# Optimization experiments

Hardware: AMD Instinct MI355X
Metric: run time of the kernel (lower is better)

Reference implementation:

```python
import jax, jax.numpy as jnp
import numpy as np

V, E, H, O = 32000, 512, 1024, 8   # vocab, embed_dim, hidden_dim, output_dim
B, T = 64, 512
PAD = 1  # padding_idx=1 in nn.Embedding


def setup_inputs() -> dict:
    key = jax.random.key(0)
    ks = jax.random.split(key, 8)
    s = 1.0 / np.sqrt(H)  # torch LSTM init scale
    x = jax.random.randint(ks[0], (B, T), 0, V)
    W_emb = jax.random.normal(ks[1], (V, E), dtype=jnp.float32)
    W_emb = W_emb.at[PAD].set(0.0)  # padding row is zero
    W_ih = jax.random.uniform(ks[2], (4 * H, E), jnp.float32, -s, s)
    W_hh = jax.random.uniform(ks[3], (4 * H, H), jnp.float32, -s, s)
    b_ih = jax.random.uniform(ks[4], (4 * H,), jnp.float32, -s, s)
    b_hh = jax.random.uniform(ks[5], (4 * H,), jnp.float32, -s, s)
    W_out = jax.random.uniform(ks[6], (O, H), jnp.float32, -s, s)
    b_out = jax.random.uniform(ks[7], (O,), jnp.float32, -s, s)
    return {"x": x, "W_emb": W_emb, "W_ih": W_ih, "W_hh": W_hh,
            "b_ih": b_ih, "b_hh": b_hh, "W_out": W_out, "b_out": b_out}


def _lstm_scan(emb_tbe, W_ih, W_hh, b_ih, b_hh):
    # emb_tbe: [T, B, E] -> hidden states [T, B, H]; torch gate order i,f,g,o
    Hh = W_hh.shape[1]
    b = b_ih + b_hh

    def step(carry, x_t):
        h, c = carry
        z = x_t @ W_ih.T + h @ W_hh.T + b  # [B, 4H]
        i, f, g, o = jnp.split(z, 4, axis=-1)
        c = jax.nn.sigmoid(f) * c + jax.nn.sigmoid(i) * jnp.tanh(g)
        h = jax.nn.sigmoid(o) * jnp.tanh(c)
        return (h, c), h

    h0 = jnp.zeros((emb_tbe.shape[1], Hh), emb_tbe.dtype)
    _, hs = jax.lax.scan(step, (h0, h0), emb_tbe)
    return hs


def reference(x, W_emb, W_ih, W_hh, b_ih, b_hh, W_out, b_out):
    Bsz = x.shape[0]
    emb = W_emb[x]                                   # [B, T, E]
    hs = _lstm_scan(emb.transpose(1, 0, 2), W_ih, W_hh, b_ih, b_hh)
    outputs = hs.transpose(1, 0, 2)                  # [B, T, H]
    pad = (x == PAD)
    outputs = jnp.where(pad[..., None], 0.0, outputs)  # masked_fill_
    lengths = jnp.sum(~pad, axis=1)                  # non-pad token counts
    final = outputs[jnp.arange(Bsz), lengths - 1]    # [B, H]
    # Dropout(p=0.5) is identity in eval mode
    logits = final @ W_out.T + b_out                 # [B, O]
    return logits
```

## Files before the change

kernel.cpp:

```cpp
#include <hip/hip_runtime.h>

typedef short bf16x8 __attribute__((ext_vector_type(8)));
typedef float f32x4  __attribute__((ext_vector_type(4)));
typedef unsigned long long u64;

#define MFMA16(a, b, c) __builtin_amdgcn_mfma_f32_16x16x32_bf16((a), (b), (c), 0, 0, 0)
#define AT_LD(p, o)    __hip_atomic_load((p), (o), __HIP_MEMORY_SCOPE_AGENT)
#define AT_ST(p, v, o) __hip_atomic_store((p), (v), (o), __HIP_MEMORY_SCOPE_AGENT)
#define AT_ADD(p, v, o) __hip_atomic_fetch_add((p), (v), (o), __HIP_MEMORY_SCOPE_AGENT)

#define HSLOT 67584

__device__ __forceinline__ unsigned short f2bf(float f) {
  union { float f; unsigned u; } v; v.f = f;
  unsigned u = v.u;
  u += 0x7fffu + ((u >> 16) & 1u);
  return (unsigned short)(u >> 16);
}
__device__ __forceinline__ float bf2f(unsigned short h) {
  union { unsigned u; float f; } v; v.u = ((unsigned)h) << 16;
  return v.f;
}
__device__ __forceinline__ float sigf(float x) { return 1.f / (1.f + __expf(-x)); }
__device__ __forceinline__ float tanh_(float x) {
  x = fminf(15.f, fmaxf(-15.f, x));
  float e = __expf(2.f * x);
  return (e - 1.f) / (e + 1.f);
}

__device__ __forceinline__ void gbar_rec(unsigned* bar, int wg, unsigned target) {
  __syncthreads();
  if (threadIdx.x == 0) {
    asm volatile("" ::: "memory");
    unsigned arr = AT_ADD(bar + (wg & 3) * 64, 1u, __ATOMIC_RELAXED);
    if (arr == target * 32u - 1u) {
      unsigned rarr = AT_ADD(bar + 256, 1u, __ATOMIC_RELAXED);
      if (rarr == target * 4u - 1u) AT_ST(bar + 320, target, __ATOMIC_RELAXED);
    }
    while (AT_LD(bar + 320, __ATOMIC_RELAXED) < target) __builtin_amdgcn_s_sleep(1);
    asm volatile("" ::: "memory");
  }
  __syncthreads();
}

__device__ __forceinline__ void gbar_gemm(unsigned* bar, unsigned target) {
  __syncthreads();
  if (threadIdx.x == 0) {
    unsigned arr = AT_ADD(bar + 384, 1u, __ATOMIC_RELEASE);
    if (arr == target * 128u - 1u) AT_ST(bar + 448, target, __ATOMIC_RELEASE);
    while (AT_LD(bar + 448, __ATOMIC_RELAXED) < target) __builtin_amdgcn_s_sleep(4);
    asm volatile("" ::: "memory");
  }
  __syncthreads();
}

__global__ void k_conv(const float* __restrict__ wih, const float* __restrict__ whh,
                       const float* __restrict__ wemb,
                       unsigned short* __restrict__ oih, unsigned short* __restrict__ ohh,
                       unsigned short* __restrict__ oemb) {
  const size_t NIH = (size_t)4096 * 512, NHH = (size_t)4096 * 1024;
  const size_t NE = (size_t)32000 * 512;
  size_t i0 = ((size_t)blockIdx.x * blockDim.x + threadIdx.x) * 4;
  size_t gs = (size_t)gridDim.x * blockDim.x * 4;
  for (size_t j = i0; j < NIH; j += gs) {
    float4 v = *(const float4*)(wih + j);
    uint2 pk;
    pk.x = (unsigned)f2bf(v.x) | ((unsigned)f2bf(v.y) << 16);
    pk.y = (unsigned)f2bf(v.z) | ((unsigned)f2bf(v.w) << 16);
    *(uint2*)(oih + j) = pk;
  }
  for (size_t j = i0; j < NHH; j += gs) {
    float4 v = *(const float4*)(whh + j);
    uint2 pk;
    pk.x = (unsigned)f2bf(v.x) | ((unsigned)f2bf(v.y) << 16);
    pk.y = (unsigned)f2bf(v.z) | ((unsigned)f2bf(v.w) << 16);
    *(uint2*)(ohh + j) = pk;
  }
  if (oemb)
    for (size_t j = i0; j < NE; j += gs) {
      float4 v = *(const float4*)(wemb + j);
      uint2 pk;
      pk.x = (unsigned)f2bf(v.x) | ((unsigned)f2bf(v.y) << 16);
      pk.y = (unsigned)f2bf(v.z) | ((unsigned)f2bf(v.w) << 16);
      *(uint2*)(oemb + j) = pk;
    }
}

__global__ void k_tsel(const int* __restrict__ x, int* __restrict__ tsel,
                       int* __restrict__ padsel) {
  int b = threadIdx.x >> 3, j = threadIdx.x & 7;
  int c = 0;
  for (int t = j * 64; t < j * 64 + 64; ++t) c += (x[b * 512 + t] != 1) ? 1 : 0;
  c += __shfl_xor(c, 1);
  c += __shfl_xor(c, 2);
  c += __shfl_xor(c, 4);
  if (j == 0) {
    int ts = (c - 1) & 511;
    tsel[b] = ts;
    padsel[b] = (x[b * 512 + ts] == 1) ? 1 : 0;
  }
}

__global__ void k_logits(const float* __restrict__ finalb, const float* __restrict__ Wout,
                         const float* __restrict__ bout, float* __restrict__ out) {
  int tid = threadIdx.x;
  for (int e = tid; e < 512; e += 256) {
    int b = e >> 3, o = e & 7;
    const float* f = finalb + (size_t)b * 1024;
    const float* w = Wout + (size_t)o * 1024;
    float s = 0.f;
    for (int k = 0; k < 1024; ++k) s += f[k] * w[k];
    out[e] = s + bout[o];
  }
}

struct SmemT {
  unsigned short sW[32][1032];
  union {
    struct { unsigned short A[128][72]; unsigned short Bt[256][72]; } g;
    struct { float z[64][33]; } rec;
    struct { unsigned short zs[128][136]; } zst;
  } u;
};

__global__ __launch_bounds__(256, 1) void k_main(
    const int* __restrict__ x, const float* __restrict__ Wemb,
    const float* __restrict__ bih, const float* __restrict__ bhh,
    const unsigned short* __restrict__ Wihb, const unsigned short* __restrict__ Whhb,
    const unsigned short* __restrict__ wembb,
    unsigned short* __restrict__ hr, float* __restrict__ finalb,
    const int* __restrict__ tsel, const int* __restrict__ padsel,
    unsigned short* __restrict__ zxr, unsigned* __restrict__ bar, int chunkT,
    int fullzx) {
  __shared__ SmemT smem;
  const int wg = blockIdx.x, tid = threadIdx.x;
  const int wave = tid >> 6, lane = tid & 63;
  const int l15 = lane & 15, lg = lane >> 4;
  unsigned* gemm_done = bar + 512;
  unsigned* rec_done  = bar + 576;

  const f32x4 fz = {0.f, 0.f, 0.f, 0.f};
  const int nChunks = 512 / chunkT;
  const size_t slotE = (size_t)chunkT * 64 * 4096;

  if (wg < 128) {
    for (int e = tid; e < 32 * 128; e += 256) {
      int n = e >> 7;
      int kq = (e & 127) << 3;
      int grow = (n >> 3) * 1024 + wg * 8 + (n & 7);
      *(uint4*)&smem.sW[n][kq] = *(const uint4*)(Whhb + (size_t)grow * 1024 + kq);
    }
    const int q = tid & 3;
    const int my_b = tid >> 2;
    const int zc = wg * 8 + 2 * q;
    float biasv[4][2];
#pragma unroll
    for (int g = 0; g < 4; ++g)
#pragma unroll
      for (int c = 0; c < 2; ++c) biasv[g][c] = bih[g * 1024 + zc + c] + bhh[g * 1024 + zc + c];
    const int my_tsel = tsel[my_b];
    const int my_pad = padsel[my_b];
    const size_t hwe = (size_t)((my_b >> 4) * 32 + (wg >> 2)) * 512 +
                       (size_t)(wg & 3) * 128 + (size_t)(my_b & 15) * 8 + 2 * q;
    float cc0 = 0.f, cc1 = 0.f;
    unsigned bt = 0;

    AT_ST((unsigned*)hr + (wg * 256 + tid), 0u, __ATOMIC_RELAXED);
    gbar_rec(bar, wg, ++bt);

    for (int ch = 0; ch < nChunks; ++ch) {
      const int t0 = ch * chunkT;
      const unsigned short* zxbase =
          zxr + (fullzx ? (size_t)ch * slotE : (size_t)(ch & 1) * slotE);

      if (tid == 0) {
        while (AT_LD(gemm_done, __ATOMIC_RELAXED) < (unsigned)(ch + 1))
          __builtin_amdgcn_s_sleep(4);
        (void)AT_LD(gemm_done, __ATOMIC_ACQUIRE);
        asm volatile("" ::: "memory");
      }
      __syncthreads();

      union { uint2 u2[2]; unsigned short s[8]; } vv;
      {
        const unsigned short* zr = zxbase + (size_t)my_b * 4096 + zc * 4;
        vv.u2[0] = *(const uint2*)zr;
        vv.u2[1] = *(const uint2*)(zr + 4);
      }

      for (int tl = 0; tl < chunkT; ++tl) {
        const int t = t0 + tl;

        const unsigned short* hp =
            hr + (size_t)(t & 15) * HSLOT + (size_t)wave * 16384 + (size_t)lane * 8;
        f32x4 r0 = fz, r1 = fz;
        bf16x8 af[32];
#pragma unroll
        for (int j = 0; j < 32; ++j) af[j] = *(const bf16x8*)(hp + (size_t)j * 512);
#pragma unroll
        for (int j = 0; j < 32; ++j) {
          int ks = j * 32;
          bf16x8 b0 = *(const bf16x8*)&smem.sW[l15][ks + (lg << 3)];
          bf16x8 b1 = *(const bf16x8*)&smem.sW[16 + l15][ks + (lg << 3)];
          r0 = MFMA16(af[j], b0, r0);
          r1 = MFMA16(af[j], b1, r1);
        }
#pragma unroll
        for (int r = 0; r < 4; ++r) {
          smem.u.rec.z[wave * 16 + (lg << 2) + r][l15] = r0[r];
          smem.u.rec.z[wave * 16 + (lg << 2) + r][16 + l15] = r1[r];
        }
        __syncthreads();

        int hc = 2 * q;
        float zi0 = smem.u.rec.z[my_b][hc]          + biasv[0][0] + bf2f(vv.s[0]);
        float zf0 = smem.u.rec.z[my_b][8 + hc]      + biasv[1][0] + bf2f(vv.s[1]);
        float zg0 = smem.u.rec.z[my_b][16 + hc]     + biasv[2][0] + bf2f(vv.s[2]);
        float zo0 = smem.u.rec.z[my_b][24 + hc]     + biasv[3][0] + bf2f(vv.s[3]);
        float zi1 = smem.u.rec.z[my_b][hc + 1]      + biasv[0][1] + bf2f(vv.s[4]);
        float zf1 = smem.u.rec.z[my_b][8 + hc + 1]  + biasv[1][1] + bf2f(vv.s[5]);
        float zg1 = smem.u.rec.z[my_b][16 + hc + 1] + biasv[2][1] + bf2f(vv.s[6]);
        float zo1 = smem.u.rec.z[my_b][24 + hc + 1] + biasv[3][1] + bf2f(vv.s[7]);

        cc0 = sigf(zf0) * cc0 + sigf(zi0) * tanh_(zg0);
        cc1 = sigf(zf1) * cc1 + sigf(zi1) * tanh_(zg1);
        float h0 = sigf(zo0) * tanh_(cc0);
        float h1 = sigf(zo1) * tanh_(cc1);

        if (t == my_tsel) {
          finalb[(size_t)my_b * 1024 + zc]     = my_pad ? 0.f : h0;
          finalb[(size_t)my_b * 1024 + zc + 1] = my_pad ? 0.f : h1;
        }
        unsigned hp32 = (unsigned)f2bf(h0) | ((unsigned)f2bf(h1) << 16);
        AT_ST((unsigned*)(hr + (size_t)((t + 1) & 15) * HSLOT + hwe), hp32,
              __ATOMIC_RELAXED);

        if (tl + 1 < chunkT) {
          const unsigned short* zn =
              zxbase + (size_t)((tl + 1) * 64 + my_b) * 4096 + zc * 4;
          vv.u2[0] = *(const uint2*)zn;
          vv.u2[1] = *(const uint2*)(zn + 4);
        }
        gbar_rec(bar, wg, ++bt);
      }
      if (!fullzx && wg == 0 && tid == 0)
        AT_ST(rec_done, (unsigned)(ch + 1), __ATOMIC_RELAXED);
    }
  } else {
    const int gw = wg - 128;
    unsigned gt = 0;
    for (int ch = 0; ch < nChunks; ++ch) {
      if (!fullzx && tid == 0 && ch >= 2) {
        while (AT_LD(rec_done, __ATOMIC_RELAXED) < (unsigned)(ch - 1))
          __builtin_amdgcn_s_sleep(4);
        asm volatile("" ::: "memory");
      }
      __syncthreads();

      const int t0 = ch * chunkT;
      unsigned short* zx = zxr + (fullzx ? (size_t)ch * slotE : (size_t)(ch & 1) * slotE);
      const int pmN = chunkT >> 1;
      const int npatch = pmN * 16;

      for (int p = gw; p < npatch; p += 128) {
        const int pm = p % pmN;
        const int n0 = (p / pmN) * 256;
        f32x4 acc[8][4];
#pragma unroll
        for (int mt = 0; mt < 8; ++mt)
#pragma unroll
          for (int nt = 0; nt < 4; ++nt) acc[mt][nt] = fz;

        for (int kc = 0; kc < 512; kc += 64) {
          __syncthreads();
          {
            int r = tid >> 1, half = (tid & 1) << 5;
            int tl = pm * 2 + (r >> 6), b = r & 63;
            int erow = x[b * 512 + t0 + tl];
            if (wembb) {
              const unsigned short* srcp = wembb + (size_t)erow * 512 + kc + half;
#pragma unroll
              for (int j = 0; j < 32; j += 8)
                *(uint4*)&smem.u.g.A[r][half + j] = *(const uint4*)(srcp + j);
            } else {
              const float* srcp = Wemb + (size_t)erow * 512 + kc + half;
#pragma unroll
              for (int j = 0; j < 32; j += 4) {
                float4 v = *(const float4*)(srcp + j);
                uint2 pk;
                pk.x = (unsigned)f2bf(v.x) | ((unsigned)f2bf(v.y) << 16);
                pk.y = (unsigned)f2bf(v.z) | ((unsigned)f2bf(v.w) << 16);
                *(uint2*)&smem.u.g.A[r][half + j] = pk;
              }
            }
          }
          {
            int zcx = n0 + tid;
            int wrow = (zcx & 3) * 1024 + (zcx >> 2);
            const unsigned short* srcp = Wihb + (size_t)wrow * 512 + kc;
#pragma unroll
            for (int j = 0; j < 64; j += 8)
              *(uint4*)&smem.u.g.Bt[tid][j] = *(const uint4*)(srcp + j);
          }
          __syncthreads();
#pragma unroll
          for (int ks = 0; ks < 64; ks += 32) {
            bf16x8 af[8];
#pragma unroll
            for (int mt = 0; mt < 8; ++mt)
              af[mt] = *(const bf16x8*)&smem.u.g.A[mt * 16 + l15][ks + (lg << 3)];
#pragma unroll
            for (int nt = 0; nt < 4; ++nt) {
              bf16x8 bfr =
                  *(const bf16x8*)&smem.u.g.Bt[(wave * 4 + nt) * 16 + l15][ks + (lg << 3)];
#pragma unroll
              for (int mt = 0; mt < 8; ++mt)
                acc[mt][nt] = MFMA16(af[mt], bfr, acc[mt][nt]);
            }
          }
        }
#pragma unroll
        for (int h = 0; h < 2; ++h) {
          __syncthreads();
          if ((wave >> 1) == h) {
#pragma unroll
            for (int mt = 0; mt < 8; ++mt)
#pragma unroll
              for (int nt = 0; nt < 4; ++nt)
#pragma unroll
                for (int r = 0; r < 4; ++r)
                  smem.u.zst.zs[mt * 16 + (lg << 2) + r][(wave & 1) * 64 + nt * 16 + l15] =
                      f2bf(acc[mt][nt][r]);
          }
          __syncthreads();
          int m = tid >> 1, qq = (tid & 1) << 6;
          int tl2 = pm * 2 + (m >> 6), bb = m & 63;
          unsigned short* dst = zx + ((size_t)(tl2 * 64 + bb)) * 4096 + n0 + h * 128 + qq;
#pragma unroll
          for (int j = 0; j < 64; j += 8)
            *(uint4*)(dst + j) = *(const uint4*)&smem.u.zst.zs[m][qq + j];
        }
      }
      gbar_gemm(bar, ++gt);
      if (wg == 128 && tid == 0) AT_ST(gemm_done, gt, __ATOMIC_RELAXED);
    }
  }
}

extern "C" void kernel_launch(void* const* d_in, const int* in_sizes, int n_in,
                              void* d_out, int out_size, void* d_ws, size_t ws_size,
                              hipStream_t stream) {
  (void)in_sizes; (void)n_in; (void)out_size;
  const int*   x    = (const int*)  d_in[0];
  const float* Wemb = (const float*)d_in[1];
  const float* Wih  = (const float*)d_in[2];
  const float* Whh  = (const float*)d_in[3];
  const float* bih  = (const float*)d_in[4];
  const float* bhh  = (const float*)d_in[5];
  const float* Wout = (const float*)d_in[6];
  const float* bout = (const float*)d_in[7];
  float* out = (float*)d_out;
  char* ws = (char*)d_ws;

  constexpr size_t OFF_WIH = 0;
  constexpr size_t OFF_WHH = OFF_WIH + (size_t)4096 * 512 * 2;
  constexpr size_t OFF_HR  = OFF_WHH + (size_t)4096 * 1024 * 2;
  constexpr size_t OFF_FIN = OFF_HR + (size_t)16 * HSLOT * 2;
  constexpr size_t OFF_TS  = OFF_FIN + (size_t)64 * 1024 * 4;
  constexpr size_t OFF_PS  = OFF_TS + 4096;
  constexpr size_t OFF_BAR = OFF_PS + 4096;
  constexpr size_t OFF_WEB = OFF_BAR + 4096;
  constexpr size_t WEB_SZ  = (size_t)32000 * 512 * 2;
  constexpr size_t ZX_FULL = (size_t)512 * 64 * 4096 * 2;

  int chunkT = 16;
  bool wbf = true;
  int fullzx = 0;
  if (OFF_WEB + WEB_SZ + ZX_FULL <= ws_size) {
    fullzx = 1;
  } else if (OFF_WEB + WEB_SZ + (size_t)2 * 16 * 64 * 4096 * 2 <= ws_size) {
  } else if (OFF_WEB + (size_t)2 * 16 * 64 * 4096 * 2 <= ws_size) {
    wbf = false;
  } else {
    wbf = false;
    while (chunkT > 2 &&
           OFF_WEB + (size_t)2 * chunkT * 64 * 4096 * 2 > ws_size)
      chunkT >>= 1;
  }
  const size_t OFF_ZX = OFF_WEB + (wbf ? WEB_SZ : 0);

  unsigned short* wihb  = (unsigned short*)(ws + OFF_WIH);
  unsigned short* whhb  = (unsigned short*)(ws + OFF_WHH);
  unsigned short* hr    = (unsigned short*)(ws + OFF_HR);
  float* finalb         = (float*)(ws + OFF_FIN);
  int* tsel             = (int*)(ws + OFF_TS);
  int* padsel           = (int*)(ws + OFF_PS);
  unsigned* bar         = (unsigned*)(ws + OFF_BAR);
  unsigned short* wembb = wbf ? (unsigned short*)(ws + OFF_WEB) : (unsigned short*)nullptr;
  unsigned short* zxr   = (unsigned short*)(ws + OFF_ZX);

  hipMemsetAsync(ws + OFF_BAR, 0, 4096, stream);
  k_conv<<<2048, 256, 0, stream>>>(Wih, Whh, Wemb, wihb, whhb, wembb);
  k_tsel<<<1, 512, 0, stream>>>(x, tsel, padsel);
  k_main<<<256, 256, 0, stream>>>(x, Wemb, bih, bhh, wihb, whhb, wembb, hr, finalb,
                                  tsel, padsel, zxr, bar, chunkT, fullzx);
  k_logits<<<1, 256, 0, stream>>>(finalb, Wout, bout, out);
}
```

Before: 3.322 ms.

## Split input GEMM into separate kernel and use flag-based recurrence barrier

When the workspace can hold the full input-projection buffer, the embedding×W_ih GEMM now runs as its own 256-block kernel ahead of a dedicated 128-block recurrence kernel, replacing the fused producer/consumer kernel. The recurrence uses a new barrier in which each block writes a per-block flag and block 0 gathers them and publishes a generation counter, replacing the hierarchical atomic-add barrier. An acquire load is issued only once every 16 steps. This aims to cut per-step barrier latency and remove GEMM interference with the serial recurrence, at the cost of losing overlap between the GEMM and the recurrence and relying on weak memory ordering.

```diff
diff --git a/kernel.cpp b/kernel.cpp
--- a/kernel.cpp
+++ b/kernel.cpp
@@ -26,6 +26,33 @@
   x = fminf(15.f, fmaxf(-15.f, x));
   float e = __expf(2.f * x);
   return (e - 1.f) / (e + 1.f);
+}
+
+__device__ __forceinline__ void flagbar(unsigned* bar, int wg, unsigned target,
+                                        int do_acq) {
+  unsigned* gen = bar + 8192;
+  __syncthreads();
+  if (threadIdx.x == 0) {
+    asm volatile("" ::: "memory");
+    AT_ST(bar + wg * 64, target, __ATOMIC_RELAXED);
+  }
+  if (wg == 0) {
+    if (threadIdx.x < 128) {
+      while (AT_LD(bar + threadIdx.x * 64, __ATOMIC_RELAXED) < target)
+        __builtin_amdgcn_s_sleep(1);
+    }
+    __syncthreads();
+    if (threadIdx.x == 0) AT_ST(gen, target, __ATOMIC_RELAXED);
+  } else {
+    if (threadIdx.x == 0) {
+      while (AT_LD(gen, __ATOMIC_RELAXED) < target) __builtin_amdgcn_s_sleep(1);
+    }
+  }
+  if (do_acq && threadIdx.x == 0) {
+    (void)AT_LD(gen, __ATOMIC_ACQUIRE);
+    asm volatile("" ::: "memory");
+  }
+  __syncthreads();
 }
 
 __device__ __forceinline__ void gbar_rec(unsigned* bar, int wg, unsigned target) {
@@ -42,7 +69,6 @@
   }
   __syncthreads();
 }
-
 __device__ __forceinline__ void gbar_gemm(unsigned* bar, unsigned target) {
   __syncthreads();
   if (threadIdx.x == 0) {
@@ -114,6 +140,211 @@
   }
 }
 
+struct GSmem {
+  union {
+    struct { unsigned short A[128][72]; unsigned short Bt[256][72]; } g;
+    struct { unsigned short zs[128][136]; } zst;
+  } u;
+  unsigned short pad[14336];
+};
+
+__global__ __launch_bounds__(256, 1) void k_gemm(
+    const int* __restrict__ x, const float* __restrict__ Wemb,
+    const unsigned short* __restrict__ Wihb, const unsigned short* __restrict__ wembb,
+    unsigned short* __restrict__ zxr) {
+  __shared__ GSmem smem;
+  const int wg = blockIdx.x, tid = threadIdx.x;
+  const int wave = tid >> 6, lane = tid & 63;
+  const int l15 = lane & 15, lg = lane >> 4;
+  if (tid == 65535) smem.pad[0] = 0;
+  const f32x4 fz = {0.f, 0.f, 0.f, 0.f};
+  const int pmN = 256, npatch = pmN * 16;
+
+  for (int p = wg; p < npatch; p += 256) {
+    const int pm = p % pmN;
+    const int n0 = (p / pmN) * 256;
+    f32x4 acc[8][4];
+#pragma unroll
+    for (int mt = 0; mt < 8; ++mt)
+#pragma unroll
+      for (int nt = 0; nt < 4; ++nt) acc[mt][nt] = fz;
+
+    for (int kc = 0; kc < 512; kc += 64) {
+      __syncthreads();
+      {
+        int r = tid >> 1, half = (tid & 1) << 5;
+        int t = pm * 2 + (r >> 6), b = r & 63;
+        int erow = x[b * 512 + t];
+        if (wembb) {
+          const unsigned short* srcp = wembb + (size_t)erow * 512 + kc + half;
+#pragma unroll
+          for (int j = 0; j < 32; j += 8)
+            *(uint4*)&smem.u.g.A[r][half + j] = *(const uint4*)(srcp + j);
+        } else {
+          const float* srcp = Wemb + (size_t)erow * 512 + kc + half;
+#pragma unroll
+          for (int j = 0; j < 32; j += 4) {
+            float4 v = *(const float4*)(srcp + j);
+            uint2 pk;
+            pk.x = (unsigned)f2bf(v.x) | ((unsigned)f2bf(v.y) << 16);
+            pk.y = (unsigned)f2bf(v.z) | ((unsigned)f2bf(v.w) << 16);
+            *(uint2*)&smem.u.g.A[r][half + j] = pk;
+          }
+        }
+      }
+      {
+        int zcx = n0 + tid;
+        int wrow = (zcx & 3) * 1024 + (zcx >> 2);
+        const unsigned short* srcp = Wihb + (size_t)wrow * 512 + kc;
+#pragma unroll
+        for (int j = 0; j < 64; j += 8)
+          *(uint4*)&smem.u.g.Bt[tid][j] = *(const uint4*)(srcp + j);
+      }
+      __syncthreads();
+#pragma unroll
+      for (int ks = 0; ks < 64; ks += 32) {
+        bf16x8 af[8];
+#pragma unroll
+        for (int mt = 0; mt < 8; ++mt)
+          af[mt] = *(const bf16x8*)&smem.u.g.A[mt * 16 + l15][ks + (lg << 3)];
+#pragma unroll
+        for (int nt = 0; nt < 4; ++nt) {
+          bf16x8 bfr =
+              *(const bf16x8*)&smem.u.g.Bt[(wave * 4 + nt) * 16 + l15][ks + (lg << 3)];
+#pragma unroll
+          for (int mt = 0; mt < 8; ++mt)
+            acc[mt][nt] = MFMA16(af[mt], bfr, acc[mt][nt]);
+        }
+      }
+    }
+#pragma unroll
+    for (int h = 0; h < 2; ++h) {
+      __syncthreads();
+      if ((wave >> 1) == h) {
+#pragma unroll
+        for (int mt = 0; mt < 8; ++mt)
+#pragma unroll
+          for (int nt = 0; nt < 4; ++nt)
+#pragma unroll
+            for (int r = 0; r < 4; ++r)
+              smem.u.zst.zs[mt * 16 + (lg << 2) + r][(wave & 1) * 64 + nt * 16 + l15] =
+                  f2bf(acc[mt][nt][r]);
+      }
+      __syncthreads();
+      int m = tid >> 1, qq = (tid & 1) << 6;
+      int t2 = pm * 2 + (m >> 6), bb = m & 63;
+      unsigned short* dst = zxr + ((size_t)(t2 * 64 + bb)) * 4096 + n0 + h * 128 + qq;
+#pragma unroll
+      for (int j = 0; j < 64; j += 8)
+        *(uint4*)(dst + j) = *(const uint4*)&smem.u.zst.zs[m][qq + j];
+    }
+  }
+}
+
+struct RSmem {
+  unsigned short sW[32][1032];
+  float z[64][33];
+  unsigned short pad[5120];
+};
+
+__global__ __launch_bounds__(256, 1) void k_rec(
+    const float* __restrict__ bih, const float* __restrict__ bhh,
+    const unsigned short* __restrict__ Whhb,
+    unsigned short* __restrict__ hr, float* __restrict__ finalb,
+    const int* __restrict__ tsel, const int* __restrict__ padsel,
+    const unsigned short* __restrict__ zxr, unsigned* __restrict__ bar) {
+  __shared__ RSmem smem;
+  const int wg = blockIdx.x, tid = threadIdx.x;
+  const int wave = tid >> 6, lane = tid & 63;
+  const int l15 = lane & 15, lg = lane >> 4;
+  if (tid == 65535) smem.pad[0] = 0;
+  const f32x4 fz = {0.f, 0.f, 0.f, 0.f};
+
+  for (int e = tid; e < 32 * 128; e += 256) {
+    int n = e >> 7, kq = (e & 127) << 3;
+    int grow = (n >> 3) * 1024 + wg * 8 + (n & 7);
+    *(uint4*)&smem.sW[n][kq] = *(const uint4*)(Whhb + (size_t)grow * 1024 + kq);
+  }
+  const int q = tid & 3;
+  const int my_b = tid >> 2;
+  const int zc = wg * 8 + 2 * q;
+  float biasv[4][2];
+#pragma unroll
+  for (int g = 0; g < 4; ++g)
+#pragma unroll
+    for (int c = 0; c < 2; ++c)
+      biasv[g][c] = bih[g * 1024 + zc + c] + bhh[g * 1024 + zc + c];
+  const int my_tsel = tsel[my_b];
+  const int my_pad = padsel[my_b];
+  const size_t hwe = (size_t)((my_b >> 4) * 32 + (wg >> 2)) * 512 +
+                     (size_t)(wg & 3) * 128 + (size_t)(my_b & 15) * 8 + 2 * q;
+  float cc0 = 0.f, cc1 = 0.f;
+  unsigned bt = 0;
+
+  AT_ST((unsigned*)hr + (wg * 256 + tid), 0u, __ATOMIC_RELAXED);
+  flagbar(bar, wg, ++bt, 0);
+
+  union { uint2 u2[2]; unsigned short s[8]; } vv;
+  {
+    const unsigned short* zr = zxr + (size_t)my_b * 4096 + zc * 4;
+    vv.u2[0] = *(const uint2*)zr;
+    vv.u2[1] = *(const uint2*)(zr + 4);
+  }
+
+  for (int t = 0; t < 512; ++t) {
+    const unsigned short* hp =
+        hr + (size_t)(t & 15) * HSLOT + (size_t)wave * 16384 + (size_t)lane * 8;
+    f32x4 r0 = fz, r1 = fz;
+    bf16x8 af[32];
+#pragma unroll
+    for (int j = 0; j < 32; ++j) af[j] = *(const bf16x8*)(hp + (size_t)j * 512);
+#pragma unroll
+    for (int j = 0; j < 32; ++j) {
+      int ks = j * 32;
+      bf16x8 b0 = *(const bf16x8*)&smem.sW[l15][ks + (lg << 3)];
+      bf16x8 b1 = *(const bf16x8*)&smem.sW[16 + l15][ks + (lg << 3)];
+      r0 = MFMA16(af[j], b0, r0);
+      r1 = MFMA16(af[j], b1, r1);
+    }
+#pragma unroll
+    for (int r = 0; r < 4; ++r) {
+      smem.z[wave * 16 + (lg << 2) + r][l15] = r0[r];
+      smem.z[wave * 16 + (lg << 2) + r][16 + l15] = r1[r];
+    }
+    __syncthreads();
+
+    int hc = 2 * q;
+    float zi0 = smem.z[my_b][hc]          + biasv[0][0] + bf2f(vv.s[0]);
+    float zf0 = smem.z[my_b][8 + hc]      + biasv[1][0] + bf2f(vv.s[1]);
+    float zg0 = smem.z[my_b][16 + hc]     + biasv[2][0] + bf2f(vv.s[2]);
+    float zo0 = smem.z[my_b][24 + hc]     + biasv[3][0] + bf2f(vv.s[3]);
+    float zi1 = smem.z[my_b][hc + 1]      + biasv[0][1] + bf2f(vv.s[4]);
+    float zf1 = smem.z[my_b][8 + hc + 1]  + biasv[1][1] + bf2f(vv.s[5]);
+    float zg1 = smem.z[my_b][16 + hc + 1] + biasv[2][1] + bf2f(vv.s[6]);
+    float zo1 = smem.z[my_b][24 + hc + 1] + biasv[3][1] + bf2f(vv.s[7]);
+
+    cc0 = sigf(zf0) * cc0 + sigf(zi0) * tanh_(zg0);
+    cc1 = sigf(zf1) * cc1 + sigf(zi1) * tanh_(zg1);
+    float h0 = sigf(zo0) * tanh_(cc0);
+    float h1 = sigf(zo1) * tanh_(cc1);
+
+    if (t == my_tsel) {
+      finalb[(size_t)my_b * 1024 + zc]     = my_pad ? 0.f : h0;
+      finalb[(size_t)my_b * 1024 + zc + 1] = my_pad ? 0.f : h1;
+    }
+    unsigned hp32 = (unsigned)f2bf(h0) | ((unsigned)f2bf(h1) << 16);
+    AT_ST((unsigned*)(hr + (size_t)((t + 1) & 15) * HSLOT + hwe), hp32,
+          __ATOMIC_RELAXED);
+
+    if (t + 1 < 512) {
+      const unsigned short* zn = zxr + ((size_t)(t + 1) * 64 + my_b) * 4096 + zc * 4;
+      vv.u2[0] = *(const uint2*)zn;
+      vv.u2[1] = *(const uint2*)(zn + 4);
+    }
+    flagbar(bar, wg, ++bt, (t & 15) == 6);
+  }
+}
+
 struct SmemT {
   unsigned short sW[32][1032];
   union {
@@ -130,23 +361,20 @@
     const unsigned short* __restrict__ wembb,
     unsigned short* __restrict__ hr, float* __restrict__ finalb,
     const int* __restrict__ tsel, const int* __restrict__ padsel,
-    unsigned short* __restrict__ zxr, unsigned* __restrict__ bar, int chunkT,
-    int fullzx) {
+    unsigned short* __restrict__ zxr, unsigned* __restrict__ bar, int chunkT) {
   __shared__ SmemT smem;
   const int wg = blockIdx.x, tid = threadIdx.x;
   const int wave = tid >> 6, lane = tid & 63;
   const int l15 = lane & 15, lg = lane >> 4;
   unsigned* gemm_done = bar + 512;
   unsigned* rec_done  = bar + 576;
-
   const f32x4 fz = {0.f, 0.f, 0.f, 0.f};
   const int nChunks = 512 / chunkT;
   const size_t slotE = (size_t)chunkT * 64 * 4096;
 
   if (wg < 128) {
     for (int e = tid; e < 32 * 128; e += 256) {
-      int n = e >> 7;
-      int kq = (e & 127) << 3;
+      int n = e >> 7, kq = (e & 127) << 3;
       int grow = (n >> 3) * 1024 + wg * 8 + (n & 7);
       *(uint4*)&smem.sW[n][kq] = *(const uint4*)(Whhb + (size_t)grow * 1024 + kq);
     }
@@ -157,22 +385,20 @@
 #pragma unroll
     for (int g = 0; g < 4; ++g)
 #pragma unroll
-      for (int c = 0; c < 2; ++c) biasv[g][c] = bih[g * 1024 + zc + c] + bhh[g * 1024 + zc + c];
+      for (int c = 0; c < 2; ++c)
+        biasv[g][c] = bih[g * 1024 + zc + c] + bhh[g * 1024 + zc + c];
     const int my_tsel = tsel[my_b];
     const int my_pad = padsel[my_b];
     const size_t hwe = (size_t)((my_b >> 4) * 32 + (wg >> 2)) * 512 +
                        (size_t)(wg & 3) * 128 + (size_t)(my_b & 15) * 8 + 2 * q;
     float cc0 = 0.f, cc1 = 0.f;
     unsigned bt = 0;
-
     AT_ST((unsigned*)hr + (wg * 256 + tid), 0u, __ATOMIC_RELAXED);
     gbar_rec(bar, wg, ++bt);
 
     for (int ch = 0; ch < nChunks; ++ch) {
       const int t0 = ch * chunkT;
-      const unsigned short* zxbase =
-          zxr + (fullzx ? (size_t)ch * slotE : (size_t)(ch & 1) * slotE);
-
+      const unsigned short* zxbase = zxr + (size_t)(ch & 1) * slotE;
       if (tid == 0) {
         while (AT_LD(gemm_done, __ATOMIC_RELAXED) < (unsigned)(ch + 1))
           __builtin_amdgcn_s_sleep(4);
@@ -180,17 +406,14 @@
         asm volatile("" ::: "memory");
       }
       __syncthreads();
-
       union { uint2 u2[2]; unsigned short s[8]; } vv;
       {
         const unsigned short* zr = zxbase + (size_t)my_b * 4096 + zc * 4;
         vv.u2[0] = *(const uint2*)zr;
         vv.u2[1] = *(const uint2*)(zr + 4);
       }
-
       for (int tl = 0; tl < chunkT; ++tl) {
         const int t = t0 + tl;
-
         const unsigned short* hp =
             hr + (size_t)(t & 15) * HSLOT + (size_t)wave * 16384 + (size_t)lane * 8;
         f32x4 r0 = fz, r1 = fz;
@@ -211,7 +434,6 @@
           smem.u.rec.z[wave * 16 + (lg << 2) + r][16 + l15] = r1[r];
         }
         __syncthreads();
-
         int hc = 2 * q;
         float zi0 = smem.u.rec.z[my_b][hc]          + biasv[0][0] + bf2f(vv.s[0]);
         float zf0 = smem.u.rec.z[my_b][8 + hc]      + biasv[1][0] + bf2f(vv.s[1]);
@@ -221,12 +443,10 @@
         float zf1 = smem.u.rec.z[my_b][8 + hc + 1]  + biasv[1][1] + bf2f(vv.s[5]);
         float zg1 = smem.u.rec.z[my_b][16 + hc + 1] + biasv[2][1] + bf2f(vv.s[6]);
         float zo1 = smem.u.rec.z[my_b][24 + hc + 1] + biasv[3][1] + bf2f(vv.s[7]);
-
         cc0 = sigf(zf0) * cc0 + sigf(zi0) * tanh_(zg0);
         cc1 = sigf(zf1) * cc1 + sigf(zi1) * tanh_(zg1);
         float h0 = sigf(zo0) * tanh_(cc0);
         float h1 = sigf(zo1) * tanh_(cc1);
-
         if (t == my_tsel) {
           finalb[(size_t)my_b * 1024 + zc]     = my_pad ? 0.f : h0;
           finalb[(size_t)my_b * 1024 + zc + 1] = my_pad ? 0.f : h1;
@@ -234,7 +454,6 @@
         unsigned hp32 = (unsigned)f2bf(h0) | ((unsigned)f2bf(h1) << 16);
         AT_ST((unsigned*)(hr + (size_t)((t + 1) & 15) * HSLOT + hwe), hp32,
               __ATOMIC_RELAXED);
-
         if (tl + 1 < chunkT) {
           const unsigned short* zn =
               zxbase + (size_t)((tl + 1) * 64 + my_b) * 4096 + zc * 4;
@@ -243,25 +462,22 @@
         }
         gbar_rec(bar, wg, ++bt);
       }
-      if (!fullzx && wg == 0 && tid == 0)
-        AT_ST(rec_done, (unsigned)(ch + 1), __ATOMIC_RELAXED);
+      if (wg == 0 && tid == 0) AT_ST(rec_done, (unsigned)(ch + 1), __ATOMIC_RELAXED);
     }
   } else {
     const int gw = wg - 128;
     unsigned gt = 0;
     for (int ch = 0; ch < nChunks; ++ch) {
-      if (!fullzx && tid == 0 && ch >= 2) {
+      if (tid == 0 && ch >= 2) {
         while (AT_LD(rec_done, __ATOMIC_RELAXED) < (unsigned)(ch - 1))
           __builtin_amdgcn_s_sleep(4);
         asm volatile("" ::: "memory");
       }
       __syncthreads();
-
       const int t0 = ch * chunkT;
-      unsigned short* zx = zxr + (fullzx ? (size_t)ch * slotE : (size_t)(ch & 1) * slotE);
+      unsigned short* zx = zxr + (size_t)(ch & 1) * slotE;
       const int pmN = chunkT >> 1;
       const int npatch = pmN * 16;
-
       for (int p = gw; p < npatch; p += 128) {
         const int pm = p % pmN;
         const int n0 = (p / pmN) * 256;
@@ -270,7 +486,6 @@
         for (int mt = 0; mt < 8; ++mt)
 #pragma unroll
           for (int nt = 0; nt < 4; ++nt) acc[mt][nt] = fz;
-
         for (int kc = 0; kc < 512; kc += 64) {
           __syncthreads();
           {
@@ -369,23 +584,22 @@
   constexpr size_t OFF_TS  = OFF_FIN + (size_t)64 * 1024 * 4;
   constexpr size_t OFF_PS  = OFF_TS + 4096;
   constexpr size_t OFF_BAR = OFF_PS + 4096;
-  constexpr size_t OFF_WEB = OFF_BAR + 4096;
+  constexpr size_t OFF_WEB = OFF_BAR + 40960;
   constexpr size_t WEB_SZ  = (size_t)32000 * 512 * 2;
   constexpr size_t ZX_FULL = (size_t)512 * 64 * 4096 * 2;
 
+  bool split = (OFF_WEB + WEB_SZ + ZX_FULL <= ws_size);
   int chunkT = 16;
   bool wbf = true;
-  int fullzx = 0;
-  if (OFF_WEB + WEB_SZ + ZX_FULL <= ws_size) {
-    fullzx = 1;
-  } else if (OFF_WEB + WEB_SZ + (size_t)2 * 16 * 64 * 4096 * 2 <= ws_size) {
-  } else if (OFF_WEB + (size_t)2 * 16 * 64 * 4096 * 2 <= ws_size) {
-    wbf = false;
-  } else {
-    wbf = false;
-    while (chunkT > 2 &&
-           OFF_WEB + (size_t)2 * chunkT * 64 * 4096 * 2 > ws_size)
-      chunkT >>= 1;
+  if (!split) {
+    if (OFF_WEB + WEB_SZ + (size_t)2 * 16 * 64 * 4096 * 2 <= ws_size) {
+    } else if (OFF_WEB + (size_t)2 * 16 * 64 * 4096 * 2 <= ws_size) {
+      wbf = false;
+    } else {
+      wbf = false;
+      while (chunkT > 2 && OFF_WEB + (size_t)2 * chunkT * 64 * 4096 * 2 > ws_size)
+        chunkT >>= 1;
+    }
   }
   const size_t OFF_ZX = OFF_WEB + (wbf ? WEB_SZ : 0);
 
@@ -399,10 +613,15 @@
   unsigned short* wembb = wbf ? (unsigned short*)(ws + OFF_WEB) : (unsigned short*)nullptr;
   unsigned short* zxr   = (unsigned short*)(ws + OFF_ZX);
 
-  hipMemsetAsync(ws + OFF_BAR, 0, 4096, stream);
+  hipMemsetAsync(ws + OFF_BAR, 0, 40960, stream);
   k_conv<<<2048, 256, 0, stream>>>(Wih, Whh, Wemb, wihb, whhb, wembb);
   k_tsel<<<1, 512, 0, stream>>>(x, tsel, padsel);
-  k_main<<<256, 256, 0, stream>>>(x, Wemb, bih, bhh, wihb, whhb, wembb, hr, finalb,
-                                  tsel, padsel, zxr, bar, chunkT, fullzx);
+  if (split) {
+    k_gemm<<<256, 256, 0, stream>>>(x, Wemb, wihb, wembb, zxr);
+    k_rec<<<128, 256, 0, stream>>>(bih, bhh, whhb, hr, finalb, tsel, padsel, zxr, bar);
+  } else {
+    k_main<<<256, 256, 0, stream>>>(x, Wemb, bih, bhh, wihb, whhb, wembb, hr, finalb,
+                                    tsel, padsel, zxr, bar, chunkT);
+  }
   k_logits<<<1, 256, 0, stream>>>(finalb, Wout, bout, out);
 }
```

Measured after the change: 3.326 ms. Within noise of the previous version (+0.1%).

## Replace atomic-counter grid barrier with per-WG flags and ring of zx slots

Applied to the files above, without the earlier changes.

The recurrent-step grid barrier changes from a hierarchical atomic-add counter to per-workgroup flag stores. Workgroup 0 polls all 128 flags and then publishes a generation word that the other workgroups spin on. The input-projection buffer becomes a ring of up to 32 slots sized from the workspace, replacing the full-or-double-buffer choice, and the GEMM workgroups wait on rec_done only when the ring wraps. The goal is to cut per-timestep barrier latency and atomic contention, at the cost of a serial gather step through workgroup 0 and a larger barrier area.

```diff
diff --git a/kernel.cpp b/kernel.cpp
--- a/kernel.cpp
+++ b/kernel.cpp
@@ -28,17 +28,24 @@
   return (e - 1.f) / (e + 1.f);
 }
 
-__device__ __forceinline__ void gbar_rec(unsigned* bar, int wg, unsigned target) {
+__device__ __forceinline__ void flagbar(unsigned* bar, int wg, unsigned target) {
+  unsigned* gen = bar + 8192;
   __syncthreads();
   if (threadIdx.x == 0) {
     asm volatile("" ::: "memory");
-    unsigned arr = AT_ADD(bar + (wg & 3) * 64, 1u, __ATOMIC_RELAXED);
-    if (arr == target * 32u - 1u) {
-      unsigned rarr = AT_ADD(bar + 256, 1u, __ATOMIC_RELAXED);
-      if (rarr == target * 4u - 1u) AT_ST(bar + 320, target, __ATOMIC_RELAXED);
-    }
-    while (AT_LD(bar + 320, __ATOMIC_RELAXED) < target) __builtin_amdgcn_s_sleep(1);
-    asm volatile("" ::: "memory");
+    AT_ST(bar + wg * 64, target, __ATOMIC_RELAXED);
+  }
+  if (wg == 0) {
+    if (threadIdx.x < 128) {
+      while (AT_LD(bar + threadIdx.x * 64, __ATOMIC_RELAXED) < target)
+        __builtin_amdgcn_s_sleep(1);
+    }
+    __syncthreads();
+    if (threadIdx.x == 0) AT_ST(gen, target, __ATOMIC_RELAXED);
+  } else {
+    if (threadIdx.x == 0) {
+      while (AT_LD(gen, __ATOMIC_RELAXED) < target) __builtin_amdgcn_s_sleep(1);
+    }
   }
   __syncthreads();
 }
@@ -46,9 +53,9 @@
 __device__ __forceinline__ void gbar_gemm(unsigned* bar, unsigned target) {
   __syncthreads();
   if (threadIdx.x == 0) {
-    unsigned arr = AT_ADD(bar + 384, 1u, __ATOMIC_RELEASE);
-    if (arr == target * 128u - 1u) AT_ST(bar + 448, target, __ATOMIC_RELEASE);
-    while (AT_LD(bar + 448, __ATOMIC_RELAXED) < target) __builtin_amdgcn_s_sleep(4);
+    unsigned arr = AT_ADD(bar + 8256, 1u, __ATOMIC_RELEASE);
+    if (arr == target * 128u - 1u) AT_ST(bar + 8320, target, __ATOMIC_RELEASE);
+    while (AT_LD(bar + 8320, __ATOMIC_RELAXED) < target) __builtin_amdgcn_s_sleep(4);
     asm volatile("" ::: "memory");
   }
   __syncthreads();
@@ -131,22 +138,20 @@
     unsigned short* __restrict__ hr, float* __restrict__ finalb,
     const int* __restrict__ tsel, const int* __restrict__ padsel,
     unsigned short* __restrict__ zxr, unsigned* __restrict__ bar, int chunkT,
-    int fullzx) {
+    int nslot) {
   __shared__ SmemT smem;
   const int wg = blockIdx.x, tid = threadIdx.x;
   const int wave = tid >> 6, lane = tid & 63;
   const int l15 = lane & 15, lg = lane >> 4;
-  unsigned* gemm_done = bar + 512;
-  unsigned* rec_done  = bar + 576;
-
+  unsigned* gemm_done = bar + 8384;
+  unsigned* rec_done  = bar + 8448;
   const f32x4 fz = {0.f, 0.f, 0.f, 0.f};
   const int nChunks = 512 / chunkT;
   const size_t slotE = (size_t)chunkT * 64 * 4096;
 
   if (wg < 128) {
     for (int e = tid; e < 32 * 128; e += 256) {
-      int n = e >> 7;
-      int kq = (e & 127) << 3;
+      int n = e >> 7, kq = (e & 127) << 3;
       int grow = (n >> 3) * 1024 + wg * 8 + (n & 7);
       *(uint4*)&smem.sW[n][kq] = *(const uint4*)(Whhb + (size_t)grow * 1024 + kq);
     }
@@ -157,40 +162,35 @@
 #pragma unroll
     for (int g = 0; g < 4; ++g)
 #pragma unroll
-      for (int c = 0; c < 2; ++c) biasv[g][c] = bih[g * 1024 + zc + c] + bhh[g * 1024 + zc + c];
+      for (int c = 0; c < 2; ++c)
+        biasv[g][c] = bih[g * 1024 + zc + c] + bhh[g * 1024 + zc + c];
     const int my_tsel = tsel[my_b];
     const int my_pad = padsel[my_b];
     const size_t hwe = (size_t)((my_b >> 4) * 32 + (wg >> 2)) * 512 +
                        (size_t)(wg & 3) * 128 + (size_t)(my_b & 15) * 8 + 2 * q;
     float cc0 = 0.f, cc1 = 0.f;
     unsigned bt = 0;
-
     AT_ST((unsigned*)hr + (wg * 256 + tid), 0u, __ATOMIC_RELAXED);
-    gbar_rec(bar, wg, ++bt);
+    flagbar(bar, wg, ++bt);
 
     for (int ch = 0; ch < nChunks; ++ch) {
       const int t0 = ch * chunkT;
-      const unsigned short* zxbase =
-          zxr + (fullzx ? (size_t)ch * slotE : (size_t)(ch & 1) * slotE);
-
+      const unsigned short* zxbase = zxr + (size_t)(ch % nslot) * slotE;
       if (tid == 0) {
         while (AT_LD(gemm_done, __ATOMIC_RELAXED) < (unsigned)(ch + 1))
-          __builtin_amdgcn_s_sleep(4);
+          __builtin_amdgcn_s_sleep(2);
         (void)AT_LD(gemm_done, __ATOMIC_ACQUIRE);
         asm volatile("" ::: "memory");
       }
       __syncthreads();
-
       union { uint2 u2[2]; unsigned short s[8]; } vv;
       {
         const unsigned short* zr = zxbase + (size_t)my_b * 4096 + zc * 4;
         vv.u2[0] = *(const uint2*)zr;
         vv.u2[1] = *(const uint2*)(zr + 4);
       }
-
       for (int tl = 0; tl < chunkT; ++tl) {
         const int t = t0 + tl;
-
         const unsigned short* hp =
             hr + (size_t)(t & 15) * HSLOT + (size_t)wave * 16384 + (size_t)lane * 8;
         f32x4 r0 = fz, r1 = fz;
@@ -211,7 +211,6 @@
           smem.u.rec.z[wave * 16 + (lg << 2) + r][16 + l15] = r1[r];
         }
         __syncthreads();
-
         int hc = 2 * q;
         float zi0 = smem.u.rec.z[my_b][hc]          + biasv[0][0] + bf2f(vv.s[0]);
         float zf0 = smem.u.rec.z[my_b][8 + hc]      + biasv[1][0] + bf2f(vv.s[1]);
@@ -221,12 +220,10 @@
         float zf1 = smem.u.rec.z[my_b][8 + hc + 1]  + biasv[1][1] + bf2f(vv.s[5]);
         float zg1 = smem.u.rec.z[my_b][16 + hc + 1] + biasv[2][1] + bf2f(vv.s[6]);
         float zo1 = smem.u.rec.z[my_b][24 + hc + 1] + biasv[3][1] + bf2f(vv.s[7]);
-
         cc0 = sigf(zf0) * cc0 + sigf(zi0) * tanh_(zg0);
         cc1 = sigf(zf1) * cc1 + sigf(zi1) * tanh_(zg1);
         float h0 = sigf(zo0) * tanh_(cc0);
         float h1 = sigf(zo1) * tanh_(cc1);
-
         if (t == my_tsel) {
           finalb[(size_t)my_b * 1024 + zc]     = my_pad ? 0.f : h0;
           finalb[(size_t)my_b * 1024 + zc + 1] = my_pad ? 0.f : h1;
@@ -234,34 +231,30 @@
         unsigned hp32 = (unsigned)f2bf(h0) | ((unsigned)f2bf(h1) << 16);
         AT_ST((unsigned*)(hr + (size_t)((t + 1) & 15) * HSLOT + hwe), hp32,
               __ATOMIC_RELAXED);
-
         if (tl + 1 < chunkT) {
           const unsigned short* zn =
               zxbase + (size_t)((tl + 1) * 64 + my_b) * 4096 + zc * 4;
           vv.u2[0] = *(const uint2*)zn;
           vv.u2[1] = *(const uint2*)(zn + 4);
         }
-        gbar_rec(bar, wg, ++bt);
+        flagbar(bar, wg, ++bt);
       }
-      if (!fullzx && wg == 0 && tid == 0)
-        AT_ST(rec_done, (unsigned)(ch + 1), __ATOMIC_RELAXED);
+      if (wg == 0 && tid == 0) AT_ST(rec_done, (unsigned)(ch + 1), __ATOMIC_RELAXED);
     }
   } else {
     const int gw = wg - 128;
     unsigned gt = 0;
     for (int ch = 0; ch < nChunks; ++ch) {
-      if (!fullzx && tid == 0 && ch >= 2) {
-        while (AT_LD(rec_done, __ATOMIC_RELAXED) < (unsigned)(ch - 1))
-          __builtin_amdgcn_s_sleep(4);
+      if (tid == 0 && ch >= nslot) {
+        while (AT_LD(rec_done, __ATOMIC_RELAXED) < (unsigned)(ch - nslot + 1))
+          __builtin_amdgcn_s_sleep(8);
         asm volatile("" ::: "memory");
       }
       __syncthreads();
-
       const int t0 = ch * chunkT;
-      unsigned short* zx = zxr + (fullzx ? (size_t)ch * slotE : (size_t)(ch & 1) * slotE);
+      unsigned short* zx = zxr + (size_t)(ch % nslot) * slotE;
       const int pmN = chunkT >> 1;
       const int npatch = pmN * 16;
-
       for (int p = gw; p < npatch; p += 128) {
         const int pm = p % pmN;
         const int n0 = (p / pmN) * 256;
@@ -270,7 +263,6 @@
         for (int mt = 0; mt < 8; ++mt)
 #pragma unroll
           for (int nt = 0; nt < 4; ++nt) acc[mt][nt] = fz;
-
         for (int kc = 0; kc < 512; kc += 64) {
           __syncthreads();
           {
@@ -369,18 +361,20 @@
   constexpr size_t OFF_TS  = OFF_FIN + (size_t)64 * 1024 * 4;
   constexpr size_t OFF_PS  = OFF_TS + 4096;
   constexpr size_t OFF_BAR = OFF_PS + 4096;
-  constexpr size_t OFF_WEB = OFF_BAR + 4096;
+  constexpr size_t OFF_WEB = OFF_BAR + 40960;
   constexpr size_t WEB_SZ  = (size_t)32000 * 512 * 2;
-  constexpr size_t ZX_FULL = (size_t)512 * 64 * 4096 * 2;
+  constexpr size_t SLOT_SZ = (size_t)16 * 64 * 4096 * 2;
 
   int chunkT = 16;
   bool wbf = true;
-  int fullzx = 0;
-  if (OFF_WEB + WEB_SZ + ZX_FULL <= ws_size) {
-    fullzx = 1;
-  } else if (OFF_WEB + WEB_SZ + (size_t)2 * 16 * 64 * 4096 * 2 <= ws_size) {
-  } else if (OFF_WEB + (size_t)2 * 16 * 64 * 4096 * 2 <= ws_size) {
+  int nslot = 2;
+  if (OFF_WEB + WEB_SZ + 2 * SLOT_SZ <= ws_size) {
+    nslot = (int)((ws_size - OFF_WEB - WEB_SZ) / SLOT_SZ);
+    if (nslot > 32) nslot = 32;
+  } else if (OFF_WEB + 2 * SLOT_SZ <= ws_size) {
     wbf = false;
+    nslot = (int)((ws_size - OFF_WEB) / SLOT_SZ);
+    if (nslot > 32) nslot = 32;
   } else {
     wbf = false;
     while (chunkT > 2 &&
@@ -399,10 +393,10 @@
   unsigned short* wembb = wbf ? (unsigned short*)(ws + OFF_WEB) : (unsigned short*)nullptr;
   unsigned short* zxr   = (unsigned short*)(ws + OFF_ZX);
 
-  hipMemsetAsync(ws + OFF_BAR, 0, 4096, stream);
+  hipMemsetAsync(ws + OFF_BAR, 0, 40960, stream);
   k_conv<<<2048, 256, 0, stream>>>(Wih, Whh, Wemb, wihb, whhb, wembb);
   k_tsel<<<1, 512, 0, stream>>>(x, tsel, padsel);
   k_main<<<256, 256, 0, stream>>>(x, Wemb, bih, bhh, wihb, whhb, wembb, hr, finalb,
-                                  tsel, padsel, zxr, bar, chunkT, fullzx);
+                                  tsel, padsel, zxr, bar, chunkT, nslot);
   k_logits<<<1, 256, 0, stream>>>(finalb, Wout, bout, out);
 }
```

New measurement: 3.235 ms. -2.6%, faster.
